# Kernel optimization log

Measured on AMD Instinct MI355X. Metric: run time of the kernel, lower is better.

Reference implementation:

```python
import math
import jax, jax.numpy as jnp
import numpy as np

F = 8          # func_count
H = 1024       # image height (resolution)
W = 1024       # image width
N = 65536      # chaos-game points
T = 48         # iterations
WARMUP = 8     # iterations before accumulation starts


def make_rotation(theta):
    c, s = jnp.cos(theta), jnp.sin(theta)
    return jnp.stack([jnp.stack([c, -s], -1), jnp.stack([s, c], -1)], -2)


def convert_affine(inp):
    # inp: (..., 6) -> (..., 2, 3), faithful to the torch convert_affine
    sig = jax.nn.sigmoid(inp[..., :4])
    t = jnp.zeros((*inp.shape[:-1], 2, 2), inp.dtype)
    t = t.at[..., 0, 0].set(sig[..., 0] * 0.8 + 0.05)
    t = make_rotation(sig[..., 1] * (math.pi * 0.4)) @ t
    t = t.at[..., 1, 1].set(sig[..., 2] * 0.8 + 0.05)
    t = make_rotation(sig[..., 3] * (math.pi * 2.0)) @ t
    trans = (jax.nn.sigmoid(inp[..., 4:]) - 0.5) * 2.0
    return jnp.concatenate([t, trans[..., None]], axis=-1)


def setup_inputs() -> dict:
    key = jax.random.key(0)
    k1, k2, k3, k4 = jax.random.split(key, 4)
    return {
        "prob_norm": jax.random.normal(k1, (1, F, F), jnp.float32),
        "affine_params": convert_affine(jax.random.normal(k2, (1, F, 6), jnp.float32)),
        "colour_transform": jax.random.normal(k3, (1, 3, F), jnp.float32),
        "background_colour": jax.random.normal(k4, (1, 3), jnp.float32),
        "exposure": 1.0,
        "kernel_radius": 2.0,
        "gamma": 2.0,
    }


def chaos_game(affine, P, key):
    """affine: (F,2,3); P: (F,F) column-stochastic (P[next,cur]); -> hist (F,H,W)."""
    cumP = jnp.cumsum(P, axis=0)  # (F, F)
    kx, ks, kloop = jax.random.split(key, 3)
    x = jax.random.uniform(kx, (N, 2), minval=-1.0, maxval=1.0)
    s = jax.random.randint(ks, (N,), 0, F)
    hist0 = jnp.zeros((F, H, W), jnp.float32)
    keys = jax.random.split(kloop, T)

    def step(carry, inp):
        x, s, hist = carry
        t, kk = inp
        u = jax.random.uniform(kk, (N,))
        # sample next function given current state via inverse-CDF on columns
        nxt = jnp.clip(jnp.sum(cumP[:, s] < u[None, :], axis=0), 0, F - 1)
        A = affine[nxt]                                  # (N,2,3)
        x = jnp.einsum('nij,nj->ni', A[:, :, :2], x) + A[:, :, 2]
        wstep = (t >= WARMUP).astype(jnp.float32)
        # bilinear splat into [-1,1]^2 viewport
        gx = (x[:, 0] + 1.0) * 0.5 * W - 0.5
        gy = (x[:, 1] + 1.0) * 0.5 * H - 0.5
        x0 = jnp.floor(gx); y0 = jnp.floor(gy)
        fx = gx - x0; fy = gy - y0
        x0i = x0.astype(jnp.int32); y0i = y0.astype(jnp.int32)
        for dx, dy, wgt in ((0, 0, (1 - fx) * (1 - fy)), (1, 0, fx * (1 - fy)),
                            (0, 1, (1 - fx) * fy), (1, 1, fx * fy)):
            xi = x0i + dx; yi = y0i + dy
            valid = ((xi >= 0) & (xi < W) & (yi >= 0) & (yi < H)).astype(jnp.float32)
            hist = hist.at[nxt, jnp.clip(yi, 0, H - 1), jnp.clip(xi, 0, W - 1)].add(wgt * valid * wstep)
        return (x, nxt, hist), None

    (x, s, hist), _ = jax.lax.scan(step, (x, s, hist0), (jnp.arange(T), keys))
    return hist


def reference(prob_norm, affine_params, colour_transform, background_colour,
              exposure, kernel_radius, gamma):
    # convert_parameters
    P = jax.nn.sigmoid(prob_norm) + 0.001
    P = P / jnp.sum(P, axis=-2, keepdims=True)          # column-stochastic
    CT = jax.nn.sigmoid(colour_transform)                # (1,3,F)
    BG = jax.nn.sigmoid(background_colour)               # (1,3)

    hist = chaos_game(affine_params[0], P[0], jax.random.key(42))
    colour = hist[None]                                  # (1,F,H,W)
    histogram = colour.sum(1)                            # (1,H,W) == colour.sum(-3)
    colour_n = colour / (histogram[:, None] + 1e-5)

    baseline_exposure = (H * W) / float(N * (T - WARMUP))
    nexp = exposure * baseline_exposure / (kernel_radius ** 2)

    rgb = jnp.einsum('bcf,bfhw->bchw', CT, colour_n)     # (1,3,H,W)
    intensity = jnp.log1p(histogram * nexp)              # (1,H,W)
    alpha = jnp.clip(intensity, 0.0, 1.0)
    img = jnp.power(jnp.maximum(rgb * alpha[:, None], 1e-8), 1.0 / gamma)
    out = img + BG[:, :, None, None] * (1.0 - alpha[:, None])
    return out
```

## Files before the change

### kernel.cpp

```cpp
#include <hip/hip_runtime.h>
#include <hip/hip_bf16.h>
#include <math.h>


#define RNG_PARTITIONABLE 1
#define COLSUM_F32_ACCUM 1

typedef unsigned int u32;
typedef unsigned short u16;

static constexpr int FN = 8;
static constexpr int HH = 1024;
static constexpr int WW = 1024;
static constexpr int NP = 65536;
static constexpr int TI = 48;
static constexpr int WARM = 8;
static constexpr int HWPIX = HH * WW;
static constexpr int NSPLAT = TI - WARM;
static constexpr int NREC = NSPLAT * NP;
static constexpr int NBKT = 1024;
static constexpr int NBLK = NP / 256;
static constexpr u32 CHUNK = 2048;
static constexpr int MAXWG = 2304;
static constexpr int TILE_F = 2 * 1024 * 8;
static constexpr int TILE_F4 = TILE_F / 4;

static constexpr int META_CUMPT = 0;
static constexpr int META_AFF   = 64;
static constexpr int META_CT    = 112;
static constexpr int META_BG    = 136;
static constexpr int META_FLAG  = 139;
static constexpr int META_KEYS  = 140;
static constexpr int META_KX    = 236;
static constexpr int META_K2S   = 238;

struct U2 { u32 x, y; };

__device__ __forceinline__ U2 tf2x32(u32 k0, u32 k1, u32 c0, u32 c1) {
  u32 ks2 = k0 ^ k1 ^ 0x1BD11BDAu;
  u32 x0 = c0 + k0, x1 = c1 + k1;
#define TF_R(r) { x0 += x1; x1 = (x1 << (r)) | (x1 >> (32 - (r))); x1 ^= x0; }
  TF_R(13) TF_R(15) TF_R(26) TF_R(6)
  x0 += k1; x1 += ks2 + 1u;
  TF_R(17) TF_R(29) TF_R(16) TF_R(24)
  x0 += ks2; x1 += k0 + 2u;
  TF_R(13) TF_R(15) TF_R(26) TF_R(6)
  x0 += k0; x1 += k1 + 3u;
  TF_R(17) TF_R(29) TF_R(16) TF_R(24)
  x0 += k1; x1 += ks2 + 4u;
  TF_R(13) TF_R(15) TF_R(26) TF_R(6)
  x0 += ks2; x1 += k0 + 5u;
#undef TF_R
  return {x0, x1};
}

__device__ __forceinline__ u32 rbits(U2 key, u32 i, u32 halfN) {
#if RNG_PARTITIONABLE
  (void)halfN;
  U2 r = tf2x32(key.x, key.y, 0u, i);
  return r.x ^ r.y;
#else
  if (i < halfN) { U2 r = tf2x32(key.x, key.y, i, i + halfN); return r.x; }
  else           { U2 r = tf2x32(key.x, key.y, i - halfN, i); return r.y; }
#endif
}

__device__ __forceinline__ float unitf(u32 b) {
  return __uint_as_float((b >> 9) | 0x3F800000u) - 1.0f;
}

__device__ __forceinline__ float bf2f(u16 h) { return __uint_as_float(((u32)h) << 16); }
__device__ __forceinline__ float rndbf(float x) {
  u32 u = __float_as_uint(x);
  u32 r = (u + 0x7FFFu + ((u >> 16) & 1u)) & 0xFFFF0000u;
  return __uint_as_float(r);
}
__device__ __forceinline__ float rnd_m(float x, bool bf) { return bf ? rndbf(x) : x; }
__device__ __forceinline__ float ldf(const void* p, int i, bool bf) {
  return bf ? bf2f(((const u16*)p)[i]) : ((const float*)p)[i];
}
__device__ __forceinline__ float exp_cr(float x) { return (float)exp((double)x); }
__device__ __forceinline__ float sigchain(float x, bool bf) {
  float e = rnd_m(exp_cr(-x), bf);
  float d = rnd_m(1.0f + e, bf);
  return rnd_m(1.0f / d, bf);
}

__global__ __launch_bounds__(64) void setup_kernel(const void* pn, const void* affp,
                                                   const void* ctp, const void* bgp,
                                                   float* meta) {
  __shared__ int vote;
  __shared__ float sP[64];
  __shared__ u32 sroot[8];
  int tid = threadIdx.x;
  if (tid == 0) vote = 0;
  __syncthreads();
  {
    float v = fabsf(bf2f(((const u16*)pn)[tid]));
    if (v > 1e-4f && v < 16.0f) atomicAdd(&vote, 1);
  }
  __syncthreads();
  bool bf = (vote >= 50);

  if (tid == 0) {
    meta[META_FLAG] = bf ? 1.0f : 0.0f;
    u32* mu = (u32*)meta;
#if RNG_PARTITIONABLE
    U2 kx = tf2x32(0u, 42u, 0u, 0u);
    U2 ks = tf2x32(0u, 42u, 0u, 1u);
    U2 kl = tf2x32(0u, 42u, 0u, 2u);
    U2 k2 = tf2x32(ks.x, ks.y, 0u, 1u);
#else
    U2 t0 = tf2x32(0u, 42u, 0u, 3u), t1 = tf2x32(0u, 42u, 1u, 4u), t2 = tf2x32(0u, 42u, 2u, 5u);
    U2 kx{t0.x, t1.x}, ks{t2.x, t0.y}, kl{t1.y, t2.y};
    U2 r0 = tf2x32(ks.x, ks.y, 0u, 2u), r1 = tf2x32(ks.x, ks.y, 1u, 3u);
    U2 k2{r0.y, r1.y};
#endif
    sroot[0] = kx.x; sroot[1] = kx.y; sroot[2] = ks.x; sroot[3] = ks.y;
    sroot[4] = kl.x; sroot[5] = kl.y; sroot[6] = k2.x; sroot[7] = k2.y;
    mu[META_KX] = kx.x; mu[META_KX + 1] = kx.y;
    mu[META_K2S] = k2.x; mu[META_K2S + 1] = k2.y;
  }

  float c001 = bf ? 0.00099945068359375f : 0.001f;
  sP[tid] = rnd_m(sigchain(ldf(pn, tid, bf), bf) + c001, bf);
  if (tid < 48) meta[META_AFF + tid] = ldf(affp, tid, bf);
  if (tid < 24) meta[META_CT + tid] = sigchain(ldf(ctp, tid, bf), bf);
  if (tid < 3)  meta[META_BG + tid] = sigchain(ldf(bgp, tid, bf), bf);
  __syncthreads();

  if (tid < 48) {
    U2 kl{sroot[4], sroot[5]};
    u32* mu = (u32*)meta;
#if RNG_PARTITIONABLE
    U2 kt = tf2x32(kl.x, kl.y, 0u, (u32)tid);
#else
    u32 e0 = 2u * tid, e1 = 2u * tid + 1u;
    u32 w0 = (e0 < 48u) ? tf2x32(kl.x, kl.y, e0, e0 + 48u).x : tf2x32(kl.x, kl.y, e0 - 48u, e0).y;
    u32 w1 = (e1 < 48u) ? tf2x32(kl.x, kl.y, e1, e1 + 48u).x : tf2x32(kl.x, kl.y, e1 - 48u, e1).y;
    U2 kt{w0, w1};
#endif
    mu[META_KEYS + 2 * tid]     = kt.x;
    mu[META_KEYS + 2 * tid + 1] = kt.y;
  }

  if (tid < 8) {
    int c = tid;
    float a[8];
#if COLSUM_F32_ACCUM
    float cs = 0.0f;
    for (int r = 0; r < 8; ++r) cs += sP[r * 8 + c];
    cs = rnd_m(cs, bf);
#else
    float cs = 0.0f;
    for (int r = 0; r < 8; ++r) cs = rnd_m(cs + sP[r * 8 + c], bf);
#endif
    for (int r = 0; r < 8; ++r) a[r] = rnd_m(sP[r * 8 + c] / cs, bf);
    float b0 = rnd_m(a[0] + a[1], bf), b1 = rnd_m(a[2] + a[3], bf);
    float b2 = rnd_m(a[4] + a[5], bf), b3 = rnd_m(a[6] + a[7], bf);
    float c0 = rnd_m(b0 + b1, bf), c1v = rnd_m(b2 + b3, bf);
    float d0 = rnd_m(c0 + c1v, bf);
    float s5 = rnd_m(c0 + b2, bf);
    float cum[8] = { a[0], b0, rnd_m(b0 + a[2], bf), c0,
                     rnd_m(c0 + a[4], bf), s5, rnd_m(s5 + a[6], bf), d0 };
    for (int r = 0; r < 8; ++r) meta[META_CUMPT + c * 8 + r] = cum[r];
  }
}

__global__ __launch_bounds__(256) void chaos_record(const float* __restrict__ meta,
                                                    uint2* __restrict__ recU,
                                                    u32* __restrict__ counts) {
  __shared__ float cumPT[64];
  __shared__ float aff8[64];
  __shared__ u32 keyw[96];
  __shared__ u32 rk[4];
  __shared__ u32 cnt[NBKT];
  int tid = threadIdx.x;
  if (tid < 64) cumPT[tid] = meta[META_CUMPT + tid];
  if (tid < 48) aff8[(tid / 6) * 8 + (tid % 6)] = meta[META_AFF + tid];
  const u32* mu = (const u32*)meta;
  if (tid < 96) keyw[tid] = mu[META_KEYS + tid];
  if (tid < 4)  rk[tid] = mu[META_KX + tid];
  for (int b = tid; b < NBKT; b += 256) cnt[b] = 0u;
  __syncthreads();

  u32 n = blockIdx.x * 256u + (u32)tid;
  U2 kx{rk[0], rk[1]}, k2{rk[2], rk[3]};
  float x = fmaxf(-1.0f, unitf(rbits(kx, 2u * n,      65536u)) * 2.0f - 1.0f);
  float y = fmaxf(-1.0f, unitf(rbits(kx, 2u * n + 1u, 65536u)) * 2.0f - 1.0f);
  int s = (int)(rbits(k2, n, 32768u) & 7u);

  float uv[8];
#pragma unroll
  for (int j = 0; j < 8; ++j) {
    U2 kt{keyw[2 * j], keyw[2 * j + 1]};
    uv[j] = unitf(rbits(kt, n, 32768u));
  }
#pragma unroll
  for (int j = 0; j < 8; ++j) {
    float u = uv[j];
    float4 c0 = *(const float4*)&cumPT[s * 8];
    float4 c1 = *(const float4*)&cumPT[s * 8 + 4];
    int cntc = (c0.x < u) + (c0.y < u) + (c0.z < u) + (c0.w < u)
             + (c1.x < u) + (c1.y < u) + (c1.z < u) + (c1.w < u);
    int nxt = cntc < 7 ? cntc : 7;
    float4 A0 = *(const float4*)&aff8[nxt * 8];
    float4 A1 = *(const float4*)&aff8[nxt * 8 + 4];
    float xn = A0.x * x + A0.y * y + A0.z;
    float yn = A0.w * x + A1.x * y + A1.y;
    x = xn; y = yn; s = nxt;
  }

  for (int b = 1; b < 6; ++b) {
#pragma unroll
    for (int j = 0; j < 8; ++j) {
      U2 kt{keyw[16 * b + 2 * j], keyw[16 * b + 2 * j + 1]};
      uv[j] = unitf(rbits(kt, n, 32768u));
    }
#pragma unroll
    for (int j = 0; j < 8; ++j) {
      float u = uv[j];
      float4 c0 = *(const float4*)&cumPT[s * 8];
      float4 c1 = *(const float4*)&cumPT[s * 8 + 4];
      int cntc = (c0.x < u) + (c0.y < u) + (c0.z < u) + (c0.w < u)
               + (c1.x < u) + (c1.y < u) + (c1.z < u) + (c1.w < u);
      int nxt = cntc < 7 ? cntc : 7;
      float4 A0 = *(const float4*)&aff8[nxt * 8];
      float4 A1 = *(const float4*)&aff8[nxt * 8 + 4];
      float xn = A0.x * x + A0.y * y + A0.z;
      float yn = A0.w * x + A1.x * y + A1.y;
      x = xn; y = yn; s = nxt;

      float gx = (x + 1.0f) * 0.5f * 1024.0f - 0.5f;
      float gy = (y + 1.0f) * 0.5f * 1024.0f - 0.5f;
      float fx0 = floorf(gx), fy0 = floorf(gy);
      float fx = gx - fx0, fy = gy - fy0;
      int xi = (int)fx0, yi = (int)fy0;
      u32 w0 = 0u, w1 = 0xFFFFFFFFu;
      if (yi >= -1 && yi < 1024 && xi >= -1 && xi < 1024) {
        int yc = yi < 0 ? 0 : yi;
        u32 fxq = (u32)(fx * 65536.0f); if (fxq > 65535u) fxq = 65535u;
        u32 fyq = (u32)(fy * 65536.0f); if (fyq > 65535u) fyq = 65535u;
        w0 = (fxq << 16) | fyq;
        w1 = ((u32)s << 22) | ((u32)(yi + 1) << 11) | (u32)(xi + 1);
        atomicAdd(&cnt[(u32)yc], 1u);
      }
      recU[((b - 1) * 8 + j) * NP + n] = make_uint2(w0, w1);
    }
  }
  __syncthreads();
  for (int bb = tid; bb < NBKT; bb += 256) counts[bb * NBLK + blockIdx.x] = cnt[bb];
}

__global__ __launch_bounds__(256) void pre_a(u32* __restrict__ counts,
                                             u32* __restrict__ totals) {
  int bkt = blockIdx.x, tid = threadIdx.x;
  __shared__ u32 sc[256];
  u32 v = counts[bkt * NBLK + tid];
  sc[tid] = v;
  __syncthreads();
  for (int off = 1; off < 256; off <<= 1) {
    u32 t = (tid >= off) ? sc[tid - off] : 0u;
    __syncthreads();
    sc[tid] += t;
    __syncthreads();
  }
  counts[bkt * NBLK + tid] = sc[tid] - v;
  if (tid == 255) totals[bkt] = sc[tid];
}

__global__ __launch_bounds__(1024) void pre_b(const u32* __restrict__ totals,
                                              u32* __restrict__ starts) {
  int tid = threadIdx.x;
  __shared__ u32 sc[NBKT];
  u32 v = totals[tid];
  sc[tid] = v;
  __syncthreads();
  for (int off = 1; off < NBKT; off <<= 1) {
    u32 t = (tid >= off) ? sc[tid - off] : 0u;
    __syncthreads();
    sc[tid] += t;
    __syncthreads();
  }
  starts[tid] = sc[tid] - v;
  if (tid == NBKT - 1) starts[NBKT] = sc[tid];
}

__global__ __launch_bounds__(1024) void assign_k(const u32* __restrict__ starts,
                                                 u32* __restrict__ poff,
                                                 u32* __restrict__ wgmap) {
  __shared__ u32 sc[NBKT];
  int tid = threadIdx.x;
  u32 len = starts[tid + 1] - starts[tid];
  u32 np = (len + CHUNK - 1) / CHUNK;
  sc[tid] = np;
  __syncthreads();
  for (int off = 1; off < NBKT; off <<= 1) {
    u32 t = (tid >= off) ? sc[tid - off] : 0u;
    __syncthreads();
    sc[tid] += t;
    __syncthreads();
  }
  u32 excl = sc[tid] - np;
  poff[tid] = excl;
  if (tid == NBKT - 1) poff[NBKT] = sc[tid];
  u32 total = sc[NBKT - 1];
  for (u32 j = 0; j < np; ++j) wgmap[excl + j] = ((u32)tid << 16) | j;
  for (u32 i = total + (u32)tid; i < (u32)MAXWG; i += (u32)NBKT) wgmap[i] = 0xFFFFFFFFu;
}

__global__ __launch_bounds__(256) void scatter_k(const uint2* __restrict__ recU,
                                                 uint2* __restrict__ recS,
                                                 const u32* __restrict__ counts,
                                                 const u32* __restrict__ starts) {
  __shared__ u32 cur[NBKT];
  int tid = threadIdx.x, blk = blockIdx.x;
  for (int b = tid; b < NBKT; b += 256) cur[b] = starts[b] + counts[b * NBLK + blk];
  __syncthreads();
  u32 n = (u32)blk * 256u + (u32)tid;
  for (int k = 0; k < NSPLAT; ++k) {
    uint2 r = recU[k * NP + n];
    if (r.y != 0xFFFFFFFFu) {
      int yi = (int)((r.y >> 11) & 0x7FFu) - 1;
      int yc = yi < 0 ? 0 : yi;
      u32 pos = atomicAdd(&cur[(u32)yc], 1u);
      recS[pos] = r;
    }
  }
}

__global__ __launch_bounds__(256) void accum_k(const uint2* __restrict__ recS,
                                               const u32* __restrict__ starts,
                                               const u32* __restrict__ wgmap,
                                               float4* __restrict__ scratch) {
  u32 a = wgmap[blockIdx.x];
  if (a == 0xFFFFFFFFu) return;
  __shared__ float tile[TILE_F];
  int tid = threadIdx.x;
  int b = (int)(a >> 16);
  u32 j = a & 0xFFFFu;
  u32 rs = starts[b] + j * CHUNK;
  u32 re = starts[b + 1];
  u32 rlim = rs + CHUNK;
  if (rlim < re) re = rlim;

  float4* t4 = (float4*)tile;
  for (int i = tid; i < TILE_F4; i += 256) t4[i] = make_float4(0.f, 0.f, 0.f, 0.f);
  __syncthreads();

  for (u32 i = rs + (u32)tid; i < re; i += 256u) {
    uint2 r = recS[i];
    int xi = (int)(r.y & 0x7FFu) - 1;
    int yi = (int)((r.y >> 11) & 0x7FFu) - 1;
    int sfn = (int)((r.y >> 22) & 7u);
    float fx = (float)(r.x >> 16) * (1.0f / 65536.0f);
    float fy = (float)(r.x & 0xFFFFu) * (1.0f / 65536.0f);
    float ofx = 1.0f - fx, ofy = 1.0f - fy;
    bool y0ok = (u32)yi < 1024u, y1ok = (u32)(yi + 1) < 1024u;
    bool x0ok = (u32)xi < 1024u, x1ok = (u32)(xi + 1) < 1024u;
    int base = ((yi - b) * 1024 + xi) * 8 + sfn;
    if (y0ok && x0ok) atomicAdd(&tile[base],        ofx * ofy);
    if (y0ok && x1ok) atomicAdd(&tile[base + 8],    fx * ofy);
    if (y1ok && x0ok) atomicAdd(&tile[base + 8192], ofx * fy);
    if (y1ok && x1ok) atomicAdd(&tile[base + 8200], fx * fy);
  }
  __syncthreads();

  float4* dst = scratch + (size_t)blockIdx.x * TILE_F4;
  for (int i = tid; i < TILE_F4; i += 256) dst[i] = t4[i];
}

__global__ __launch_bounds__(256) void compose_k(const float4* __restrict__ scratch,
                                                 const u32* __restrict__ poff,
                                                 const float* __restrict__ meta,
                                                 float* __restrict__ out) {
  int p = blockIdx.x * 256 + threadIdx.x;
  if (p >= HWPIX) return;
  int y = p >> 10, x = p & 1023;
  float h[8];
#pragma unroll
  for (int f = 0; f < 8; ++f) h[f] = 0.0f;
  u32 k0 = poff[y], k1 = poff[y + 1];
  for (u32 k = k0; k < k1; ++k) {
    const float4* s = scratch + (size_t)k * TILE_F4 + x * 2;
    float4 a = s[0], b4 = s[1];
    h[0] += a.x; h[1] += a.y; h[2] += a.z; h[3] += a.w;
    h[4] += b4.x; h[5] += b4.y; h[6] += b4.z; h[7] += b4.w;
  }
  if (y > 0) {
    u32 g0 = poff[y - 1], g1 = poff[y];
    for (u32 k = g0; k < g1; ++k) {
      const float4* s = scratch + (size_t)k * TILE_F4 + 2048 + x * 2;
      float4 a = s[0], b4 = s[1];
      h[0] += a.x; h[1] += a.y; h[2] += a.z; h[3] += a.w;
      h[4] += b4.x; h[5] += b4.y; h[6] += b4.z; h[7] += b4.w;
    }
  }
  float hs = 0.0f;
#pragma unroll
  for (int f = 0; f < 8; ++f) hs += h[f];
  bool bf = meta[META_FLAG] != 0.0f;
  float nexp = bf ? 0.10009765625f : 0.1f;
  float denom = hs + 1e-5f;
  float alpha = fminf(fmaxf(log1pf(hs * nexp), 0.0f), 1.0f);
  float oma = 1.0f - alpha;
#pragma unroll
  for (int c = 0; c < 3; ++c) {
    float rgb = 0.0f;
#pragma unroll
    for (int f = 0; f < 8; ++f) rgb += meta[META_CT + c * 8 + f] * h[f];
    out[(size_t)c * HWPIX + p] =
        sqrtf(fmaxf((rgb / denom) * alpha, 1e-8f)) + meta[META_BG + c] * oma;
  }
}

extern "C" void kernel_launch(void* const* d_in, const int* in_sizes, int n_in,
                              void* d_out, int out_size, void* d_ws, size_t ws_size,
                              hipStream_t stream) {
  (void)in_sizes; (void)n_in; (void)out_size; (void)ws_size;
  float4* scratch = (float4*)d_ws;
  uint2* recU = (uint2*)(scratch + (size_t)MAXWG * TILE_F4);
  uint2* recS = recU + NREC;
  u32* counts = (u32*)(recS + NREC);
  u32* totals = counts + (size_t)NBKT * NBLK;
  u32* starts = totals + NBKT;
  u32* poff   = starts + 1032;
  u32* wgmap  = poff + 1032;
  float* meta = (float*)(wgmap + MAXWG);

  setup_kernel<<<1, 64, 0, stream>>>(d_in[0], d_in[1], d_in[2], d_in[3], meta);
  chaos_record<<<NBLK, 256, 0, stream>>>(meta, recU, counts);
  pre_a<<<NBKT, 256, 0, stream>>>(counts, totals);
  pre_b<<<1, NBKT, 0, stream>>>(totals, starts);
  assign_k<<<1, NBKT, 0, stream>>>(starts, poff, wgmap);
  scatter_k<<<NBLK, 256, 0, stream>>>(recU, recS, counts, starts);
  accum_k<<<MAXWG, 256, 0, stream>>>(recS, starts, wgmap, scratch);
  compose_k<<<(HWPIX + 255) / 256, 256, 0, stream>>>(scratch, poff, meta, (float*)d_out);
}
```

Measured before the change: 225.5 us.

## Recompute chaos trajectories in scatter pass instead of storing intermediate records

Drops the unsorted record buffer: a count-only pass runs the trajectory and builds per-row histograms, then a second pass reruns the same deterministic trajectory and writes records straight to their sorted positions. This saves writing and reading about 21 MB of intermediate records in exchange for running the RNG and affine iteration twice. It also merges the two single-block prefix kernels into one and doubles the accumulation chunk size, which cuts the number of accumulation workgroups.

```diff
diff --git a/kernel.cpp b/kernel.cpp
--- a/kernel.cpp
+++ b/kernel.cpp
@@ -20,8 +20,8 @@
 static constexpr int NREC = NSPLAT * NP;
 static constexpr int NBKT = 1024;
 static constexpr int NBLK = NP / 256;
-static constexpr u32 CHUNK = 2048;
-static constexpr int MAXWG = 2304;
+static constexpr u32 CHUNK = 4096;
+static constexpr int MAXWG = 1664;
 static constexpr int TILE_F = 2 * 1024 * 8;
 static constexpr int TILE_F4 = TILE_F / 4;
 
@@ -167,9 +167,62 @@
   }
 }
 
-__global__ __launch_bounds__(256) void chaos_record(const float* __restrict__ meta,
-                                                    uint2* __restrict__ recU,
-                                                    u32* __restrict__ counts) {
+#define TRAJ_BODY(EMIT)                                                        \
+  u32 n = blockIdx.x * 256u + (u32)tid;                                        \
+  U2 kx{rk[0], rk[1]}, k2{rk[2], rk[3]};                                       \
+  float x = fmaxf(-1.0f, unitf(rbits(kx, 2u * n,      65536u)) * 2.0f - 1.0f); \
+  float y = fmaxf(-1.0f, unitf(rbits(kx, 2u * n + 1u, 65536u)) * 2.0f - 1.0f); \
+  int s = (int)(rbits(k2, n, 32768u) & 7u);                                    \
+  float uv[8];                                                                 \
+  _Pragma("unroll")                                                            \
+  for (int j = 0; j < 8; ++j) {                                                \
+    U2 kt{keyw[2 * j], keyw[2 * j + 1]};                                       \
+    uv[j] = unitf(rbits(kt, n, 32768u));                                       \
+  }                                                                            \
+  _Pragma("unroll")                                                            \
+  for (int j = 0; j < 8; ++j) {                                                \
+    float u = uv[j];                                                           \
+    float4 c0 = *(const float4*)&cumPT[s * 8];                                 \
+    float4 c1 = *(const float4*)&cumPT[s * 8 + 4];                             \
+    int cntc = (c0.x < u) + (c0.y < u) + (c0.z < u) + (c0.w < u)               \
+             + (c1.x < u) + (c1.y < u) + (c1.z < u) + (c1.w < u);              \
+    int nxt = cntc < 7 ? cntc : 7;                                             \
+    float4 A0 = *(const float4*)&aff8[nxt * 8];                                \
+    float4 A1 = *(const float4*)&aff8[nxt * 8 + 4];                            \
+    float xn = A0.x * x + A0.y * y + A0.z;                                     \
+    float yn = A0.w * x + A1.x * y + A1.y;                                     \
+    x = xn; y = yn; s = nxt;                                                   \
+  }                                                                            \
+  for (int b = 1; b < 6; ++b) {                                                \
+    _Pragma("unroll")                                                          \
+    for (int j = 0; j < 8; ++j) {                                              \
+      U2 kt{keyw[16 * b + 2 * j], keyw[16 * b + 2 * j + 1]};                   \
+      uv[j] = unitf(rbits(kt, n, 32768u));                                     \
+    }                                                                          \
+    _Pragma("unroll")                                                          \
+    for (int j = 0; j < 8; ++j) {                                              \
+      float u = uv[j];                                                         \
+      float4 c0 = *(const float4*)&cumPT[s * 8];                               \
+      float4 c1 = *(const float4*)&cumPT[s * 8 + 4];                           \
+      int cntc = (c0.x < u) + (c0.y < u) + (c0.z < u) + (c0.w < u)             \
+               + (c1.x < u) + (c1.y < u) + (c1.z < u) + (c1.w < u);            \
+      int nxt = cntc < 7 ? cntc : 7;                                           \
+      float4 A0 = *(const float4*)&aff8[nxt * 8];                              \
+      float4 A1 = *(const float4*)&aff8[nxt * 8 + 4];                          \
+      float xn = A0.x * x + A0.y * y + A0.z;                                   \
+      float yn = A0.w * x + A1.x * y + A1.y;                                   \
+      x = xn; y = yn; s = nxt;                                                 \
+      float gx = (x + 1.0f) * 0.5f * 1024.0f - 0.5f;                           \
+      float gy = (y + 1.0f) * 0.5f * 1024.0f - 0.5f;                           \
+      float fx0 = floorf(gx), fy0 = floorf(gy);                                \
+      float fx = gx - fx0, fy = gy - fy0;                                      \
+      int xi = (int)fx0, yi = (int)fy0;                                        \
+      EMIT                                                                     \
+    }                                                                          \
+  }
+
+__global__ __launch_bounds__(256) void chaos_count(const float* __restrict__ meta,
+                                                   u32* __restrict__ counts) {
   __shared__ float cumPT[64];
   __shared__ float aff8[64];
   __shared__ u32 keyw[96];
@@ -184,70 +237,13 @@
   for (int b = tid; b < NBKT; b += 256) cnt[b] = 0u;
   __syncthreads();
 
-  u32 n = blockIdx.x * 256u + (u32)tid;
-  U2 kx{rk[0], rk[1]}, k2{rk[2], rk[3]};
-  float x = fmaxf(-1.0f, unitf(rbits(kx, 2u * n,      65536u)) * 2.0f - 1.0f);
-  float y = fmaxf(-1.0f, unitf(rbits(kx, 2u * n + 1u, 65536u)) * 2.0f - 1.0f);
-  int s = (int)(rbits(k2, n, 32768u) & 7u);
-
-  float uv[8];
-#pragma unroll
-  for (int j = 0; j < 8; ++j) {
-    U2 kt{keyw[2 * j], keyw[2 * j + 1]};
-    uv[j] = unitf(rbits(kt, n, 32768u));
-  }
-#pragma unroll
-  for (int j = 0; j < 8; ++j) {
-    float u = uv[j];
-    float4 c0 = *(const float4*)&cumPT[s * 8];
-    float4 c1 = *(const float4*)&cumPT[s * 8 + 4];
-    int cntc = (c0.x < u) + (c0.y < u) + (c0.z < u) + (c0.w < u)
-             + (c1.x < u) + (c1.y < u) + (c1.z < u) + (c1.w < u);
-    int nxt = cntc < 7 ? cntc : 7;
-    float4 A0 = *(const float4*)&aff8[nxt * 8];
-    float4 A1 = *(const float4*)&aff8[nxt * 8 + 4];
-    float xn = A0.x * x + A0.y * y + A0.z;
-    float yn = A0.w * x + A1.x * y + A1.y;
-    x = xn; y = yn; s = nxt;
-  }
-
-  for (int b = 1; b < 6; ++b) {
-#pragma unroll
-    for (int j = 0; j < 8; ++j) {
-      U2 kt{keyw[16 * b + 2 * j], keyw[16 * b + 2 * j + 1]};
-      uv[j] = unitf(rbits(kt, n, 32768u));
+  TRAJ_BODY({
+    (void)fx; (void)fy;
+    if (yi >= -1 && yi < 1024 && xi >= -1 && xi < 1024) {
+      int yc = yi < 0 ? 0 : yi;
+      atomicAdd(&cnt[(u32)yc], 1u);
     }
-#pragma unroll
-    for (int j = 0; j < 8; ++j) {
-      float u = uv[j];
-      float4 c0 = *(const float4*)&cumPT[s * 8];
-      float4 c1 = *(const float4*)&cumPT[s * 8 + 4];
-      int cntc = (c0.x < u) + (c0.y < u) + (c0.z < u) + (c0.w < u)
-               + (c1.x < u) + (c1.y < u) + (c1.z < u) + (c1.w < u);
-      int nxt = cntc < 7 ? cntc : 7;
-      float4 A0 = *(const float4*)&aff8[nxt * 8];
-      float4 A1 = *(const float4*)&aff8[nxt * 8 + 4];
-      float xn = A0.x * x + A0.y * y + A0.z;
-      float yn = A0.w * x + A1.x * y + A1.y;
-      x = xn; y = yn; s = nxt;
-
-      float gx = (x + 1.0f) * 0.5f * 1024.0f - 0.5f;
-      float gy = (y + 1.0f) * 0.5f * 1024.0f - 0.5f;
-      float fx0 = floorf(gx), fy0 = floorf(gy);
-      float fx = gx - fx0, fy = gy - fy0;
-      int xi = (int)fx0, yi = (int)fy0;
-      u32 w0 = 0u, w1 = 0xFFFFFFFFu;
-      if (yi >= -1 && yi < 1024 && xi >= -1 && xi < 1024) {
-        int yc = yi < 0 ? 0 : yi;
-        u32 fxq = (u32)(fx * 65536.0f); if (fxq > 65535u) fxq = 65535u;
-        u32 fyq = (u32)(fy * 65536.0f); if (fyq > 65535u) fyq = 65535u;
-        w0 = (fxq << 16) | fyq;
-        w1 = ((u32)s << 22) | ((u32)(yi + 1) << 11) | (u32)(xi + 1);
-        atomicAdd(&cnt[(u32)yc], 1u);
-      }
-      recU[((b - 1) * 8 + j) * NP + n] = make_uint2(w0, w1);
-    }
-  }
+  })
   __syncthreads();
   for (int bb = tid; bb < NBKT; bb += 256) counts[bb * NBLK + blockIdx.x] = cnt[bb];
 }
@@ -269,10 +265,12 @@
   if (tid == 255) totals[bkt] = sc[tid];
 }
 
-__global__ __launch_bounds__(1024) void pre_b(const u32* __restrict__ totals,
-                                              u32* __restrict__ starts) {
+__global__ __launch_bounds__(1024) void pre_ba(const u32* __restrict__ totals,
+                                               u32* __restrict__ starts,
+                                               u32* __restrict__ poff,
+                                               u32* __restrict__ wgmap) {
+  __shared__ u32 sc[NBKT];
   int tid = threadIdx.x;
-  __shared__ u32 sc[NBKT];
   u32 v = totals[tid];
   sc[tid] = v;
   __syncthreads();
@@ -284,15 +282,8 @@
   }
   starts[tid] = sc[tid] - v;
   if (tid == NBKT - 1) starts[NBKT] = sc[tid];
-}
-
-__global__ __launch_bounds__(1024) void assign_k(const u32* __restrict__ starts,
-                                                 u32* __restrict__ poff,
-                                                 u32* __restrict__ wgmap) {
-  __shared__ u32 sc[NBKT];
-  int tid = threadIdx.x;
-  u32 len = starts[tid + 1] - starts[tid];
-  u32 np = (len + CHUNK - 1) / CHUNK;
+  __syncthreads();
+  u32 np = (v + CHUNK - 1) / CHUNK;
   sc[tid] = np;
   __syncthreads();
   for (int off = 1; off < NBKT; off <<= 1) {
@@ -309,24 +300,34 @@
   for (u32 i = total + (u32)tid; i < (u32)MAXWG; i += (u32)NBKT) wgmap[i] = 0xFFFFFFFFu;
 }
 
-__global__ __launch_bounds__(256) void scatter_k(const uint2* __restrict__ recU,
-                                                 uint2* __restrict__ recS,
-                                                 const u32* __restrict__ counts,
-                                                 const u32* __restrict__ starts) {
+__global__ __launch_bounds__(256) void chaos_scatter(const float* __restrict__ meta,
+                                                     const u32* __restrict__ counts,
+                                                     const u32* __restrict__ starts,
+                                                     uint2* __restrict__ recS) {
+  __shared__ float cumPT[64];
+  __shared__ float aff8[64];
+  __shared__ u32 keyw[96];
+  __shared__ u32 rk[4];
   __shared__ u32 cur[NBKT];
-  int tid = threadIdx.x, blk = blockIdx.x;
-  for (int b = tid; b < NBKT; b += 256) cur[b] = starts[b] + counts[b * NBLK + blk];
-  __syncthreads();
-  u32 n = (u32)blk * 256u + (u32)tid;
-  for (int k = 0; k < NSPLAT; ++k) {
-    uint2 r = recU[k * NP + n];
-    if (r.y != 0xFFFFFFFFu) {
-      int yi = (int)((r.y >> 11) & 0x7FFu) - 1;
+  int tid = threadIdx.x;
+  if (tid < 64) cumPT[tid] = meta[META_CUMPT + tid];
+  if (tid < 48) aff8[(tid / 6) * 8 + (tid % 6)] = meta[META_AFF + tid];
+  const u32* mu = (const u32*)meta;
+  if (tid < 96) keyw[tid] = mu[META_KEYS + tid];
+  if (tid < 4)  rk[tid] = mu[META_KX + tid];
+  for (int b = tid; b < NBKT; b += 256) cur[b] = starts[b] + counts[b * NBLK + blockIdx.x];
+  __syncthreads();
+
+  TRAJ_BODY({
+    if (yi >= -1 && yi < 1024 && xi >= -1 && xi < 1024) {
       int yc = yi < 0 ? 0 : yi;
+      u32 fxq = (u32)(fx * 65536.0f); if (fxq > 65535u) fxq = 65535u;
+      u32 fyq = (u32)(fy * 65536.0f); if (fyq > 65535u) fyq = 65535u;
       u32 pos = atomicAdd(&cur[(u32)yc], 1u);
-      recS[pos] = r;
+      recS[pos] = make_uint2((fxq << 16) | fyq,
+                             ((u32)s << 22) | ((u32)(yi + 1) << 11) | (u32)(xi + 1));
     }
-  }
+  })
 }
 
 __global__ __launch_bounds__(256) void accum_k(const uint2* __restrict__ recS,
@@ -419,8 +420,7 @@
                               hipStream_t stream) {
   (void)in_sizes; (void)n_in; (void)out_size; (void)ws_size;
   float4* scratch = (float4*)d_ws;
-  uint2* recU = (uint2*)(scratch + (size_t)MAXWG * TILE_F4);
-  uint2* recS = recU + NREC;
+  uint2* recS = (uint2*)(scratch + (size_t)MAXWG * TILE_F4);
   u32* counts = (u32*)(recS + NREC);
   u32* totals = counts + (size_t)NBKT * NBLK;
   u32* starts = totals + NBKT;
@@ -429,11 +429,10 @@
   float* meta = (float*)(wgmap + MAXWG);
 
   setup_kernel<<<1, 64, 0, stream>>>(d_in[0], d_in[1], d_in[2], d_in[3], meta);
-  chaos_record<<<NBLK, 256, 0, stream>>>(meta, recU, counts);
+  chaos_count<<<NBLK, 256, 0, stream>>>(meta, counts);
   pre_a<<<NBKT, 256, 0, stream>>>(counts, totals);
-  pre_b<<<1, NBKT, 0, stream>>>(totals, starts);
-  assign_k<<<1, NBKT, 0, stream>>>(starts, poff, wgmap);
-  scatter_k<<<NBLK, 256, 0, stream>>>(recU, recS, counts, starts);
+  pre_ba<<<1, NBKT, 0, stream>>>(totals, starts, poff, wgmap);
+  chaos_scatter<<<NBLK, 256, 0, stream>>>(meta, counts, starts, recS);
   accum_k<<<MAXWG, 256, 0, stream>>>(recS, starts, wgmap, scratch);
   compose_k<<<(HWPIX + 255) / 256, 256, 0, stream>>>(scratch, poff, meta, (float*)d_out);
 }
```

Measured after the change: 225.3 us. No clear change (-0.1%).
